# Performance work log

Hardware: AMD Instinct MI355X
Metric: run time of the kernel (lower is better)

## Reference

```python
import jax, jax.numpy as jnp
import numpy as np

N, IN_DIM, OUT_DIM, H = 1024, 128, 128, 4
D = OUT_DIM // H  # head_dim = 32
NEG_SLOPE = 0.2
MASK_VAL = -1e9
LN_EPS = 1e-5


def setup_inputs() -> dict:
    key = jax.random.key(0)
    k = jax.random.split(key, 8)
    h = jax.random.normal(k[0], (N, IN_DIM), dtype=jnp.float32)
    adj = jax.random.randint(k[1], (N, N), 0, 2, dtype=jnp.int32)
    adj = adj.at[jnp.arange(N), jnp.arange(N)].set(1)  # self-loops
    s = 1.0 / np.sqrt(IN_DIM)
    W_l = jax.random.normal(k[2], (IN_DIM, OUT_DIM), dtype=jnp.float32) * s
    W_r = jax.random.normal(k[3], (IN_DIM, OUT_DIM), dtype=jnp.float32) * s
    W_v = jax.random.normal(k[4], (IN_DIM, OUT_DIM), dtype=jnp.float32) * s
    a = jax.random.normal(k[5], (D,), dtype=jnp.float32) * (1.0 / np.sqrt(D))
    ln_g = jnp.ones((OUT_DIM,), dtype=jnp.float32)
    ln_b = jnp.zeros((OUT_DIM,), dtype=jnp.float32)
    return {"h": h, "adj": adj, "W_l": W_l, "W_r": W_r, "W_v": W_v,
            "a": a, "ln_g": ln_g, "ln_b": ln_b}


def reference(h, adj, W_l, W_r, W_v, a, ln_g, ln_b):
    n = h.shape[0]
    Wlh = (h @ W_l).reshape(n, H, D)   # [N,H,D]
    Wrh = (h @ W_r).reshape(n, H, D)   # [N,H,D]
    # pairwise additive scores: pair[i,j,h,d] = Wlh[i] + Wrh[j]
    pair = Wlh[:, None, :, :] + Wrh[None, :, :, :]          # [N,N,H,D]
    pair = jnp.where(pair >= 0, pair, NEG_SLOPE * pair)      # leaky_relu(0.2)
    e = jnp.einsum('ijhd,d->ijh', pair, a)                   # [N,N,H]
    mask = (adj != 0)[:, :, None]                            # [N,N,1]
    e = jnp.where(mask, e, MASK_VAL)
    alpha = jax.nn.softmax(e, axis=1)                        # softmax over j
    v = (h @ W_v).reshape(n, H, D)                           # [N,H,D]
    agg = jnp.einsum('ijh,jhd->ihd', alpha, v).reshape(n, OUT_DIM)
    mu = jnp.mean(agg, axis=-1, keepdims=True)
    var = jnp.mean((agg - mu) ** 2, axis=-1, keepdims=True)
    y = (agg - mu) * jax.lax.rsqrt(var + LN_EPS) * ln_g + ln_b
    return jax.nn.relu(y)
```

## Files before the change

### kernel.cpp

```cpp
#include <hip/hip_runtime.h>
#include <cstdint>

typedef _Float16 f16;
typedef _Float16 f16x2 __attribute__((ext_vector_type(2)));
typedef _Float16 f16x4 __attribute__((ext_vector_type(4)));
typedef _Float16 f16x8 __attribute__((ext_vector_type(8)));
typedef float    f32x4 __attribute__((ext_vector_type(4)));
typedef unsigned short u16;
typedef unsigned int   u32;

#define LOG2E 1.44269504088896340736f

__device__ __forceinline__ f16x2 habs2(f16x2 v) {
    union { f16x2 h; u32 u; } x; x.h = v; x.u &= 0x7FFF7FFFu; return x.h;
}
#if __has_builtin(__builtin_amdgcn_fdot2)
__device__ __forceinline__ float fdot2f(f16x2 a, f16x2 b, float c) {
    return __builtin_amdgcn_fdot2(a, b, c, false);
}
#else
__device__ __forceinline__ float fdot2f(f16x2 a, f16x2 b, float c) {
    return c + (float)a.x * (float)b.x + (float)a.y * (float)b.y;
}
#endif
#if __has_builtin(__builtin_amdgcn_exp2f)
#define EXP2F __builtin_amdgcn_exp2f
#else
#define EXP2F exp2f
#endif

__global__ __launch_bounds__(64) void k0_prep(
        const float* __restrict__ Wl, const float* __restrict__ Wr,
        const float* __restrict__ Wv, const float* __restrict__ h,
        f16* __restrict__ WT, f16* __restrict__ h16) {
    int b = blockIdx.x, t = threadIdx.x;
    if (b < 384) {
        int w = b >> 7, o = b & 127;
        const float* W = (w == 0) ? Wl : ((w == 1) ? Wr : Wv);
        f16* dst = WT + (w * 128 + o) * 128;
        #pragma unroll
        for (int kk = 0; kk < 2; kk++) {
            int k = t + kk * 64;
            dst[k] = (f16)W[k * 128 + o];
        }
    } else {
        int r0 = (b - 384) * 8;
        const float* src = h + r0 * 128;
        f16* dst = h16 + r0 * 128;
        int base = t * 16;
        #pragma unroll
        for (int e = 0; e < 16; e++) dst[base + e] = (f16)src[base + e];
    }
}

__global__ __launch_bounds__(384) void k1_proj(
        const f16* __restrict__ WT, const f16* __restrict__ h16,
        f16* __restrict__ Wlh, f16* __restrict__ WrL, f16* __restrict__ VL) {
    int t = threadIdx.x;
    int i0 = blockIdx.x * 4;
    int wsel = t >> 7, col = t & 127;

    f16x2 w2[64];
    {
        const f16x2* src = (const f16x2*)(WT + t * 128);
        #pragma unroll
        for (int c2 = 0; c2 < 64; c2++) w2[c2] = src[c2];
    }
    #pragma unroll
    for (int i = 0; i < 4; i++) {
        int j = i0 + i;
        const f16x2* hr = (const f16x2*)(h16 + j * 128);
        float acc = 0.f;
        #pragma unroll
        for (int c2 = 0; c2 < 64; c2++) acc = fdot2f(hr[c2], w2[c2], acc);
        f16 hv = (f16)acc;
        if (wsel == 0) {
            Wlh[j * 128 + col] = hv;
        } else if (wsel == 1) {
            int hh = col >> 5, dd = col & 31, c = dd >> 2, l = dd & 3;
            WrL[((hh * 8 + c) * 1024 + j) * 4 + l] = hv;
        } else {
            int hh = col >> 5, dd = col & 31;
            VL[(hh * 32 + dd) * 1024 + j] = hv;
        }
    }
}

__global__ __launch_bounds__(512) void GATv2Layer_84447646974220_kernel(
        const f16* __restrict__ Wlh, const f16* __restrict__ WrL,
        const f16* __restrict__ VL,  const int* __restrict__ adj,
        const float* __restrict__ a_, const float* __restrict__ ln_g,
        const float* __restrict__ ln_b, float* __restrict__ out) {

    __shared__ __align__(16) f16 ep[4][4][1024];
    __shared__ float aggS[2][4][128];
    __shared__ float redM[2][4][4];
    __shared__ float redS[2][4][4];

    const int t    = threadIdx.x;
    const int w    = t >> 6;
    const int lane = t & 63;
    const int hh   = w & 3;
    const int half = w >> 2;
    const int i0   = blockIdx.x * 4;

    f16x2 p2[16], q2[16];
    #pragma unroll
    for (int d2 = 0; d2 < 16; d2++) {
        float a0 = a_[2 * d2], a1 = a_[2 * d2 + 1];
        f16x2 p; p.x = (f16)(0.6f * a0); p.y = (f16)(0.6f * a1);
        f16x2 q; q.x = (f16)(0.4f * a0); q.y = (f16)(0.4f * a1);
        p2[d2] = p; q2[d2] = q;
    }
    f16x2 wl2[4][16];
    #pragma unroll
    for (int ii = 0; ii < 4; ii++) {
        const f16x2* src = (const f16x2*)(Wlh + (i0 + ii) * 128 + hh * 32);
        #pragma unroll
        for (int c2 = 0; c2 < 16; c2++) wl2[ii][c2] = src[c2];
    }

    float maxE[4];
    #pragma unroll
    for (int ii = 0; ii < 4; ii++) maxE[ii] = -__builtin_inff();

    #pragma unroll 1
    for (int jb = 0; jb < 8; jb++) {
        int j = half * 512 + jb * 64 + lane;
        f16x4 wr[8];
        #pragma unroll
        for (int c = 0; c < 8; c++)
            wr[c] = *(const f16x4*)(WrL + ((hh * 8 + c) * 1024 + j) * 4);
        int am[4];
        #pragma unroll
        for (int ii = 0; ii < 4; ii++) am[ii] = adj[(i0 + ii) * 1024 + j];

        float e[4] = {0.f, 0.f, 0.f, 0.f};
        #pragma unroll
        for (int c = 0; c < 8; c++) {
            #pragma unroll
            for (int ii = 0; ii < 4; ii++) {
                f16x2 t0 = wl2[ii][2 * c]     + wr[c].lo;
                f16x2 t1 = wl2[ii][2 * c + 1] + wr[c].hi;
                e[ii] = fdot2f(p2[2 * c],     t0, e[ii]);
                e[ii] = fdot2f(q2[2 * c],     habs2(t0), e[ii]);
                e[ii] = fdot2f(p2[2 * c + 1], t1, e[ii]);
                e[ii] = fdot2f(q2[2 * c + 1], habs2(t1), e[ii]);
            }
        }
        #pragma unroll
        for (int ii = 0; ii < 4; ii++) {
            float v = am[ii] ? e[ii] : -__builtin_inff();
            maxE[ii] = fmaxf(maxE[ii], v);
            ep[hh][ii][j] = (f16)v;
        }
    }

    #pragma unroll
    for (int ii = 0; ii < 4; ii++) {
        float M = maxE[ii];
        #pragma unroll
        for (int off = 32; off > 0; off >>= 1) M = fmaxf(M, __shfl_xor(M, off));
        if (lane == 0) redM[half][hh][ii] = M;
    }
    __syncthreads();

    #pragma unroll
    for (int ii = 0; ii < 4; ii++) {
        float M = fmaxf(redM[0][hh][ii], redM[1][hh][ii]);
        f16x8 v0 = *(f16x8*)&ep[hh][ii][half * 512 + lane * 8];
        float pb[8], l = 0.f;
        #pragma unroll
        for (int e = 0; e < 8; e++) pb[e] = EXP2F(((float)v0[e] - M) * LOG2E);
        #pragma unroll
        for (int e = 0; e < 8; e++) { v0[e] = (f16)pb[e]; l += pb[e]; }
        *(f16x8*)&ep[hh][ii][half * 512 + lane * 8] = v0;
        #pragma unroll
        for (int off = 32; off > 0; off >>= 1) l += __shfl_xor(l, off);
        if (lane == 0) redS[half][hh][ii] = l;
    }
    __syncthreads();

    float lr[4];
    #pragma unroll
    for (int ii = 0; ii < 4; ii++)
        lr[ii] = 1.0f / (redS[0][hh][ii] + redS[1][hh][ii]);

    f32x4 acc0 = {0.f, 0.f, 0.f, 0.f}, acc1 = {0.f, 0.f, 0.f, 0.f};
    const int q8  = (lane >> 4) << 3;
    const int m3  = lane & 3;
    const int n15 = lane & 15;

    #pragma unroll 1
    for (int jt4 = 0; jt4 < 4; jt4++) {
        int jt = half * 4 + jt4;
        #pragma unroll
        for (int kk = 0; kk < 4; kk++) {
            int ko = jt * 128 + kk * 32 + q8;
            f16x8 af = *(const f16x8*)&ep[hh][m3][ko];
            f16x8 b0 = *(const f16x8*)(VL + (hh * 32 + n15) * 1024 + ko);
            f16x8 b1 = *(const f16x8*)(VL + (hh * 32 + 16 + n15) * 1024 + ko);
            acc0 = __builtin_amdgcn_mfma_f32_16x16x32_f16(af, b0, acc0, 0, 0, 0);
            acc1 = __builtin_amdgcn_mfma_f32_16x16x32_f16(af, b1, acc1, 0, 0, 0);
        }
    }

    if (lane < 16) {
        #pragma unroll
        for (int r = 0; r < 4; r++) {
            aggS[half][r][hh * 32 + lane]      = acc0[r] * lr[r];
            aggS[half][r][hh * 32 + 16 + lane] = acc1[r] * lr[r];
        }
    }
    __syncthreads();

    if (w < 4) {
        float x0 = aggS[0][w][lane]      + aggS[1][w][lane];
        float x1 = aggS[0][w][lane + 64] + aggS[1][w][lane + 64];
        float s = x0 + x1, sq = x0 * x0 + x1 * x1;
        #pragma unroll
        for (int off = 32; off > 0; off >>= 1) {
            s  += __shfl_xor(s, off);
            sq += __shfl_xor(sq, off);
        }
        float mean = s * (1.f / 128.f);
        float var  = sq * (1.f / 128.f) - mean * mean;
        float rs   = rsqrtf(var + 1e-5f);
        float y0 = fmaxf((x0 - mean) * rs * ln_g[lane]      + ln_b[lane],      0.f);
        float y1 = fmaxf((x1 - mean) * rs * ln_g[lane + 64] + ln_b[lane + 64], 0.f);
        out[(i0 + w) * 128 + lane]      = y0;
        out[(i0 + w) * 128 + 64 + lane] = y1;
    }
}

extern "C" void kernel_launch(void* const* d_in, const int* in_sizes, int n_in,
                              void* d_out, int out_size, void* d_ws, size_t ws_size,
                              hipStream_t stream) {
    const float* h   = (const float*)d_in[0];
    const int*   adj = (const int*)d_in[1];
    const float* Wl  = (const float*)d_in[2];
    const float* Wr  = (const float*)d_in[3];
    const float* Wv  = (const float*)d_in[4];
    const float* a_  = (const float*)d_in[5];
    const float* g_  = (const float*)d_in[6];
    const float* b_  = (const float*)d_in[7];
    float* out = (float*)d_out;

    char* ws = (char*)d_ws;
    f16* WT  = (f16*)(ws);
    f16* h16 = (f16*)(ws + 98304);
    f16* Wlh = (f16*)(ws + 360448);
    f16* WrL = (f16*)(ws + 622592);
    f16* VL  = (f16*)(ws + 884736);

    k0_prep<<<512, 64, 0, stream>>>(Wl, Wr, Wv, h, WT, h16);
    k1_proj<<<256, 384, 0, stream>>>(WT, h16, Wlh, WrL, VL);
    GATv2Layer_84447646974220_kernel<<<256, 512, 0, stream>>>(
        Wlh, WrL, VL, adj, a_, g_, b_, out);
}
```

Before: 98.26 us.

## Fuse fp16 prep into fp32 projection and split neighbors across four wave groups

Removes the separate weight-transpose/half-conversion kernel; the projection kernel now stages four h rows in shared memory and reads fp32 weights directly with coalesced column access, accumulating in fp32. The attention kernel uses 1024 threads per block, splitting the 1024 neighbors into four quarters instead of two halves, so each wave does half the score, softmax and MFMA work. Reductions across quarters go through shared memory. This drops a launch and raises per-block parallelism, at the cost of higher register pressure under the 1024-thread launch bound.

After: 101.8 us. +3.6%, slower.

```diff
diff --git a/kernel.cpp b/kernel.cpp
--- a/kernel.cpp
+++ b/kernel.cpp
@@ -1,13 +1,11 @@
 #include <hip/hip_runtime.h>
-#include <cstdint>
 
 typedef _Float16 f16;
 typedef _Float16 f16x2 __attribute__((ext_vector_type(2)));
 typedef _Float16 f16x4 __attribute__((ext_vector_type(4)));
 typedef _Float16 f16x8 __attribute__((ext_vector_type(8)));
 typedef float    f32x4 __attribute__((ext_vector_type(4)));
-typedef unsigned short u16;
-typedef unsigned int   u32;
+typedef unsigned int u32;
 
 #define LOG2E 1.44269504088896340736f
 
@@ -29,79 +27,53 @@
 #define EXP2F exp2f
 #endif
 
-__global__ __launch_bounds__(64) void k0_prep(
-        const float* __restrict__ Wl, const float* __restrict__ Wr,
-        const float* __restrict__ Wv, const float* __restrict__ h,
-        f16* __restrict__ WT, f16* __restrict__ h16) {
-    int b = blockIdx.x, t = threadIdx.x;
-    if (b < 384) {
-        int w = b >> 7, o = b & 127;
-        const float* W = (w == 0) ? Wl : ((w == 1) ? Wr : Wv);
-        f16* dst = WT + (w * 128 + o) * 128;
-        #pragma unroll
-        for (int kk = 0; kk < 2; kk++) {
-            int k = t + kk * 64;
-            dst[k] = (f16)W[k * 128 + o];
-        }
-    } else {
-        int r0 = (b - 384) * 8;
-        const float* src = h + r0 * 128;
-        f16* dst = h16 + r0 * 128;
-        int base = t * 16;
-        #pragma unroll
-        for (int e = 0; e < 16; e++) dst[base + e] = (f16)src[base + e];
-    }
-}
-
 __global__ __launch_bounds__(384) void k1_proj(
-        const f16* __restrict__ WT, const f16* __restrict__ h16,
+        const float* __restrict__ h,  const float* __restrict__ Wl,
+        const float* __restrict__ Wr, const float* __restrict__ Wv,
         f16* __restrict__ Wlh, f16* __restrict__ WrL, f16* __restrict__ VL) {
-    int t = threadIdx.x;
-    int i0 = blockIdx.x * 4;
-    int wsel = t >> 7, col = t & 127;
-
-    f16x2 w2[64];
-    {
-        const f16x2* src = (const f16x2*)(WT + t * 128);
-        #pragma unroll
-        for (int c2 = 0; c2 < 64; c2++) w2[c2] = src[c2];
-    }
+    __shared__ float hs[4][128];
+    const int t = threadIdx.x, i0 = blockIdx.x * 4;
+    for (int idx = t; idx < 512; idx += 384)
+        hs[idx >> 7][idx & 127] = h[(i0 + (idx >> 7)) * 128 + (idx & 127)];
+    __syncthreads();
+
+    const int wsel = t >> 7, col = t & 127;
+    const float* W = (wsel == 0) ? Wl : ((wsel == 1) ? Wr : Wv);
+    float a0 = 0.f, a1 = 0.f, a2 = 0.f, a3 = 0.f;
+    #pragma unroll 8
+    for (int k = 0; k < 128; k++) {
+        float wv = W[k * 128 + col];
+        a0 += hs[0][k] * wv; a1 += hs[1][k] * wv;
+        a2 += hs[2][k] * wv; a3 += hs[3][k] * wv;
+    }
+    float accs[4] = {a0, a1, a2, a3};
+    const int hh = col >> 5, dd = col & 31, c = dd >> 2, l = dd & 3;
     #pragma unroll
     for (int i = 0; i < 4; i++) {
         int j = i0 + i;
-        const f16x2* hr = (const f16x2*)(h16 + j * 128);
-        float acc = 0.f;
-        #pragma unroll
-        for (int c2 = 0; c2 < 64; c2++) acc = fdot2f(hr[c2], w2[c2], acc);
-        f16 hv = (f16)acc;
-        if (wsel == 0) {
-            Wlh[j * 128 + col] = hv;
-        } else if (wsel == 1) {
-            int hh = col >> 5, dd = col & 31, c = dd >> 2, l = dd & 3;
-            WrL[((hh * 8 + c) * 1024 + j) * 4 + l] = hv;
-        } else {
-            int hh = col >> 5, dd = col & 31;
-            VL[(hh * 32 + dd) * 1024 + j] = hv;
-        }
-    }
-}
-
-__global__ __launch_bounds__(512) void GATv2Layer_84447646974220_kernel(
+        f16 hv = (f16)accs[i];
+        if (wsel == 0)      Wlh[j * 128 + col] = hv;
+        else if (wsel == 1) WrL[((hh * 8 + c) * 1024 + j) * 4 + l] = hv;
+        else                VL[(hh * 32 + dd) * 1024 + j] = hv;
+    }
+}
+
+__global__ __launch_bounds__(1024, 4) void GATv2Layer_84447646974220_kernel(
         const f16* __restrict__ Wlh, const f16* __restrict__ WrL,
         const f16* __restrict__ VL,  const int* __restrict__ adj,
         const float* __restrict__ a_, const float* __restrict__ ln_g,
         const float* __restrict__ ln_b, float* __restrict__ out) {
 
     __shared__ __align__(16) f16 ep[4][4][1024];
-    __shared__ float aggS[2][4][128];
-    __shared__ float redM[2][4][4];
-    __shared__ float redS[2][4][4];
+    __shared__ float aggS[4][4][128];
+    __shared__ float redM[4][4][4];
+    __shared__ float redS[4][4][4];
 
     const int t    = threadIdx.x;
     const int w    = t >> 6;
     const int lane = t & 63;
     const int hh   = w & 3;
-    const int half = w >> 2;
+    const int quar = w >> 2;
     const int i0   = blockIdx.x * 4;
 
     f16x2 p2[16], q2[16];
@@ -125,8 +97,8 @@
     for (int ii = 0; ii < 4; ii++) maxE[ii] = -__builtin_inff();
 
     #pragma unroll 1
-    for (int jb = 0; jb < 8; jb++) {
-        int j = half * 512 + jb * 64 + lane;
+    for (int jb = 0; jb < 4; jb++) {
+        int j = quar * 256 + jb * 64 + lane;
         f16x4 wr[8];
         #pragma unroll
         for (int c = 0; c < 8; c++)
@@ -161,39 +133,41 @@
         float M = maxE[ii];
         #pragma unroll
         for (int off = 32; off > 0; off >>= 1) M = fmaxf(M, __shfl_xor(M, off));
-        if (lane == 0) redM[half][hh][ii] = M;
+        if (lane == 0) redM[quar][hh][ii] = M;
     }
     __syncthreads();
 
     #pragma unroll
     for (int ii = 0; ii < 4; ii++) {
-        float M = fmaxf(redM[0][hh][ii], redM[1][hh][ii]);
-        f16x8 v0 = *(f16x8*)&ep[hh][ii][half * 512 + lane * 8];
-        float pb[8], l = 0.f;
-        #pragma unroll
-        for (int e = 0; e < 8; e++) pb[e] = EXP2F(((float)v0[e] - M) * LOG2E);
-        #pragma unroll
-        for (int e = 0; e < 8; e++) { v0[e] = (f16)pb[e]; l += pb[e]; }
-        *(f16x8*)&ep[hh][ii][half * 512 + lane * 8] = v0;
+        float M = fmaxf(fmaxf(redM[0][hh][ii], redM[1][hh][ii]),
+                        fmaxf(redM[2][hh][ii], redM[3][hh][ii]));
+        f16x4 v0 = *(f16x4*)&ep[hh][ii][quar * 256 + lane * 4];
+        float pb[4], l = 0.f;
+        #pragma unroll
+        for (int e = 0; e < 4; e++) pb[e] = EXP2F(((float)v0[e] - M) * LOG2E);
+        #pragma unroll
+        for (int e = 0; e < 4; e++) { v0[e] = (f16)pb[e]; l += pb[e]; }
+        *(f16x4*)&ep[hh][ii][quar * 256 + lane * 4] = v0;
         #pragma unroll
         for (int off = 32; off > 0; off >>= 1) l += __shfl_xor(l, off);
-        if (lane == 0) redS[half][hh][ii] = l;
+        if (lane == 0) redS[quar][hh][ii] = l;
     }
     __syncthreads();
 
     float lr[4];
     #pragma unroll
     for (int ii = 0; ii < 4; ii++)
-        lr[ii] = 1.0f / (redS[0][hh][ii] + redS[1][hh][ii]);
+        lr[ii] = 1.0f / (redS[0][hh][ii] + redS[1][hh][ii] +
+                         redS[2][hh][ii] + redS[3][hh][ii]);
 
     f32x4 acc0 = {0.f, 0.f, 0.f, 0.f}, acc1 = {0.f, 0.f, 0.f, 0.f};
     const int q8  = (lane >> 4) << 3;
     const int m3  = lane & 3;
     const int n15 = lane & 15;
 
-    #pragma unroll 1
-    for (int jt4 = 0; jt4 < 4; jt4++) {
-        int jt = half * 4 + jt4;
+    #pragma unroll
+    for (int jt2 = 0; jt2 < 2; jt2++) {
+        int jt = quar * 2 + jt2;
         #pragma unroll
         for (int kk = 0; kk < 4; kk++) {
             int ko = jt * 128 + kk * 32 + q8;
@@ -208,15 +182,17 @@
     if (lane < 16) {
         #pragma unroll
         for (int r = 0; r < 4; r++) {
-            aggS[half][r][hh * 32 + lane]      = acc0[r] * lr[r];
-            aggS[half][r][hh * 32 + 16 + lane] = acc1[r] * lr[r];
+            aggS[quar][r][hh * 32 + lane]      = acc0[r] * lr[r];
+            aggS[quar][r][hh * 32 + 16 + lane] = acc1[r] * lr[r];
         }
     }
     __syncthreads();
 
     if (w < 4) {
-        float x0 = aggS[0][w][lane]      + aggS[1][w][lane];
-        float x1 = aggS[0][w][lane + 64] + aggS[1][w][lane + 64];
+        float x0 = aggS[0][w][lane]      + aggS[1][w][lane] +
+                   aggS[2][w][lane]      + aggS[3][w][lane];
+        float x1 = aggS[0][w][lane + 64] + aggS[1][w][lane + 64] +
+                   aggS[2][w][lane + 64] + aggS[3][w][lane + 64];
         float s = x0 + x1, sq = x0 * x0 + x1 * x1;
         #pragma unroll
         for (int off = 32; off > 0; off >>= 1) {
@@ -247,14 +223,11 @@
     float* out = (float*)d_out;
 
     char* ws = (char*)d_ws;
-    f16* WT  = (f16*)(ws);
-    f16* h16 = (f16*)(ws + 98304);
-    f16* Wlh = (f16*)(ws + 360448);
-    f16* WrL = (f16*)(ws + 622592);
-    f16* VL  = (f16*)(ws + 884736);
-
-    k0_prep<<<512, 64, 0, stream>>>(Wl, Wr, Wv, h, WT, h16);
-    k1_proj<<<256, 384, 0, stream>>>(WT, h16, Wlh, WrL, VL);
-    GATv2Layer_84447646974220_kernel<<<256, 512, 0, stream>>>(
+    f16* Wlh = (f16*)(ws);
+    f16* WrL = (f16*)(ws + 262144);
+    f16* VL  = (f16*)(ws + 524288);
+
+    k1_proj<<<256, 384, 0, stream>>>(h, Wl, Wr, Wv, Wlh, WrL, VL);
+    GATv2Layer_84447646974220_kernel<<<256, 1024, 0, stream>>>(
         Wlh, WrL, VL, adj, a_, g_, b_, out);
 }
```
